# Performance work log

Hardware: AMD Instinct MI355X
Metric: run time of the kernel (lower is better)

Reference implementation:

```python
import jax, jax.numpy as jnp
import numpy as np

N_NODES = 20000
N_EDGES = 640000
D = 128            # node feature dim
NUM_HEADS = 4      # = num_irreps of edge_sh (lmax=3, 0e+1o+2e+3o)
HEAD_DIM = D // NUM_HEADS
IR_DIMS = np.array([1, 3, 5, 7])  # dims of each irrep; sum = 16
AVG_NUM_NEIGHBORS = 32.0


def setup_inputs() -> dict:
    key = jax.random.key(0)
    ks = jax.random.split(key, 20)
    inp = {
        "edge_sh": jax.random.normal(ks[0], (N_EDGES, int(IR_DIMS.sum())), jnp.float32),
        "node_feats": jax.random.normal(ks[1], (N_NODES, D), jnp.float32),
        "edge_feats": jax.random.normal(ks[2], (N_EDGES, 64), jnp.float32),
        "chi_scalar": jax.random.normal(ks[3], (N_EDGES, 64), jnp.float32),
        "cutoffs": jax.random.uniform(ks[4], (N_EDGES,), jnp.float32),
        "senders": jax.random.randint(ks[5], (N_EDGES,), 0, N_NODES),
        "receivers": jax.random.randint(ks[6], (N_EDGES,), 0, N_NODES),
        # radial MLP: 64 -> 128 -> 128 (silu between)
        "W_rad1": jax.random.normal(ks[7], (64, 128), jnp.float32) / np.sqrt(64),
        "b_rad1": jnp.zeros((128,), jnp.float32),
        "W_rad2": jax.random.normal(ks[8], (128, 128), jnp.float32) / np.sqrt(128),
        "b_rad2": jnp.zeros((128,), jnp.float32),
        # spherical-scalar MLP: 64 -> 128 -> 128
        "W_sph1": jax.random.normal(ks[9], (64, 128), jnp.float32) / np.sqrt(64),
        "b_sph1": jnp.zeros((128,), jnp.float32),
        "W_sph2": jax.random.normal(ks[10], (128, 128), jnp.float32) / np.sqrt(128),
        "b_sph2": jnp.zeros((128,), jnp.float32),
        # Q/K projections, no bias
        "Wq": jax.random.normal(ks[11], (D, D), jnp.float32) / np.sqrt(D),
        "Wk": jax.random.normal(ks[12], (D, D), jnp.float32) / np.sqrt(D),
    }
    return inp


def reference(edge_sh, node_feats, edge_feats, chi_scalar, cutoffs, senders,
              receivers, W_rad1, b_rad1, W_rad2, b_rad2, W_sph1, b_sph1,
              W_sph2, b_sph2, Wq, Wk):
    silu = jax.nn.silu
    # edge filter: radial MLP + spherical-scalar MLP
    w = silu(edge_feats @ W_rad1 + b_rad1) @ W_rad2 + b_rad2      # [E, D]
    w = w + (silu(chi_scalar @ W_sph1 + b_sph1) @ W_sph2 + b_sph2)
    w = w.reshape(-1, NUM_HEADS, HEAD_DIM)                        # [E, H, hd]
    # gathered queries/keys
    q = (node_feats @ Wq).reshape(-1, NUM_HEADS, HEAD_DIM)[receivers]
    k = (node_feats @ Wk).reshape(-1, NUM_HEADS, HEAD_DIM)[senders]
    # filter-scaled attention: per-edge, per-head scalar
    alpha = (q * w * k).sum(axis=-1) * (1.0 / np.sqrt(HEAD_DIM))  # [E, H]
    alpha = alpha * cutoffs[:, None]
    # aligned_mul: broadcast per-irrep weight over each irrep's dim (mul=1)
    y = jnp.repeat(alpha, IR_DIMS, axis=-1)                       # [E, 16]
    msg = edge_sh * y
    # scatter_sum into receivers
    chi = jax.ops.segment_sum(msg, receivers, num_segments=N_NODES)
    return chi / AVG_NUM_NEIGHBORS
```

## Files before the change

kernel.cpp:

```cpp
#include <hip/hip_runtime.h>
#include <cmath>

#define NNODES 20000
#define NEDGES 640000
#define DDIM   128
#define TN     16
#define BE     64

typedef __attribute__((ext_vector_type(8))) short bf16x8;
typedef __attribute__((ext_vector_type(4))) float f32x4;
typedef __attribute__((ext_vector_type(4))) unsigned short us4;

__device__ __forceinline__ unsigned short f2bf(float x) {
    union { float f; unsigned u; } v; v.f = x;
    unsigned r = v.u + 0x7FFFu + ((v.u >> 16) & 1u);
    return (unsigned short)(r >> 16);
}
__device__ __forceinline__ float bf2f(unsigned short h) {
    union { unsigned u; float f; } v; v.u = ((unsigned)h) << 16; return v.f;
}
__device__ __forceinline__ unsigned cvtpk(float lo, float hi) {
    unsigned r;
    asm("v_cvt_pk_bf16_f32 %0, %1, %2" : "=v"(r) : "v"(lo), "v"(hi));
    return r;
}

__global__ void pack_weights(const float* __restrict__ W, unsigned short* __restrict__ dst)
{
    const int f  = blockIdx.x;
    const int kt = f >> 3, nt = f & 7;
    const int t  = threadIdx.x;
#pragma unroll
    for (int ii = 0; ii < 2; ii++) {
        const int idx  = t * 2 + ii;
        const int lane = idx >> 3, i = idx & 7;
        const int k = kt * 32 + (lane >> 4) * 8 + i;
        const int n = nt * 16 + (lane & 15);
        dst[f * 512 + idx] = f2bf(W[k * 128 + n]);
    }
}

__global__ __launch_bounds__(256) void qk_proj_kernel(
    const float* __restrict__ nf, const float* __restrict__ Wq,
    const float* __restrict__ Wk, unsigned short* __restrict__ qbuf,
    unsigned short* __restrict__ kbuf)
{
    __shared__ float s_nf[TN * DDIM];
    const int t  = threadIdx.x;
    const int n0 = blockIdx.x * TN;
    {
        const float4* src = (const float4*)(nf + (size_t)n0 * DDIM);
        float4* dst = (float4*)s_nf;
        for (int i = t; i < TN * DDIM / 4; i += 256) dst[i] = src[i];
    }
    __syncthreads();

    const int j = t & 127;
    const float* W = (t < 128) ? Wq : Wk;
    float acc[TN];
#pragma unroll
    for (int n = 0; n < TN; n++) acc[n] = 0.f;

    for (int k = 0; k < DDIM; k += 4) {
        const float w0 = W[(k + 0) * DDIM + j];
        const float w1 = W[(k + 1) * DDIM + j];
        const float w2 = W[(k + 2) * DDIM + j];
        const float w3 = W[(k + 3) * DDIM + j];
#pragma unroll
        for (int n = 0; n < TN; n++) {
            const float4 f = *(const float4*)&s_nf[n * DDIM + k];
            acc[n] = fmaf(f.w, w3, fmaf(f.z, w2, fmaf(f.y, w1, fmaf(f.x, w0, acc[n]))));
        }
    }
    unsigned short* outp = (t < 128) ? qbuf : kbuf;
    for (int n = 0; n < TN; n++) outp[(size_t)(n0 + n) * DDIM + j] = f2bf(acc[n]);
}

__global__ __launch_bounds__(256) void edge_kernel(
    const float* __restrict__ edge_sh, const float* __restrict__ cutoffs,
    const int* __restrict__ senders, const int* __restrict__ receivers,
    const float* __restrict__ edge_feats, const float* __restrict__ chi_scalar,
    const unsigned short* __restrict__ w1r, const unsigned short* __restrict__ w1s,
    const unsigned short* __restrict__ w2r, const unsigned short* __restrict__ w2s,
    const float* __restrict__ b_rad1, const float* __restrict__ b_sph1,
    const float* __restrict__ b_rad2, const float* __restrict__ b_sph2,
    const unsigned short* __restrict__ qbuf, const unsigned short* __restrict__ kbuf,
    float* __restrict__ out)
{
    __shared__ unsigned short s_a[2 * 64 * 64];
    __shared__ unsigned short s_h[64 * 128];
    __shared__ unsigned short s_p[64 * 128];
    __shared__ float s_alpha[64][4];

    char* pa = (char*)s_a;
    char* ph = (char*)s_h;
    char* pp = (char*)s_p;

    const int t  = threadIdx.x;
    const int w  = t >> 6;
    const int l  = t & 63;
    const int eb = blockIdx.x * BE;

#pragma unroll
    for (int ii = 0; ii < 8; ii++) {
        const int e  = w * 16 + ii * 2 + (l >> 5);
        const int eg = eb + e;
        const int r  = receivers[eg];
        const int s  = senders[eg];
        const int c4 = l & 31;
        const us4 qv = *(const us4*)(qbuf + (size_t)r * 128 + c4 * 4);
        const us4 kv = *(const us4*)(kbuf + (size_t)s * 128 + c4 * 4);
        const float p0 = bf2f(qv[0]) * bf2f(kv[0]);
        const float p1 = bf2f(qv[1]) * bf2f(kv[1]);
        const float p2 = bf2f(qv[2]) * bf2f(kv[2]);
        const float p3 = bf2f(qv[3]) * bf2f(kv[3]);
        const uint2 pv = { cvtpk(p0, p1), cvtpk(p2, p3) };
        *(uint2*)(pp + ((e * 256 + c4 * 8) ^ ((e & 7) << 4))) = pv;
    }

#pragma unroll
    for (int ii = 0; ii < 4; ii++) {
        const int idx = t + ii * 256;
        const int r   = idx >> 4;
        const int c4  = idx & 15;
        const float4 a = *(const float4*)(edge_feats + (size_t)(eb + r) * 64 + c4 * 4);
        const float4 b = *(const float4*)(chi_scalar + (size_t)(eb + r) * 64 + c4 * 4);
        const uint2 av = { cvtpk(a.x, a.y), cvtpk(a.z, a.w) };
        const uint2 bv = { cvtpk(b.x, b.y), cvtpk(b.z, b.w) };
        const int off = (r * 128 + c4 * 8) ^ ((r & 7) << 4);
        *(uint2*)(pa + off)        = av;
        *(uint2*)(pa + 8192 + off) = bv;
    }
    __syncthreads();

    f32x4 acc2[2][4];
#pragma unroll
    for (int ct = 0; ct < 2; ct++)
#pragma unroll
        for (int et = 0; et < 4; et++)
            acc2[ct][et] = (f32x4){0.f, 0.f, 0.f, 0.f};

#pragma unroll
    for (int path = 0; path < 2; path++) {
        const unsigned short* W1p = path ? w1s : w1r;
        const unsigned short* W2p = path ? w2s : w2r;
        const float* b1p = path ? b_sph1 : b_rad1;
        const char*  ab  = pa + path * 8192;

        f32x4 acc1[2][4];
#pragma unroll
        for (int ht = 0; ht < 2; ht++)
#pragma unroll
            for (int et = 0; et < 4; et++)
                acc1[ht][et] = (f32x4){0.f, 0.f, 0.f, 0.f};

#pragma unroll
        for (int kt = 0; kt < 2; kt++) {
            bf16x8 bfrag[4];
#pragma unroll
            for (int et = 0; et < 4; et++) {
                const int e = et * 16 + (l & 15);
                const int k = kt * 32 + (l >> 4) * 8;
                bfrag[et] = *(const bf16x8*)(ab + ((e * 128 + k * 2) ^ ((e & 7) << 4)));
            }
#pragma unroll
            for (int ht = 0; ht < 2; ht++) {
                const int f = kt * 8 + (w * 2 + ht);
                const bf16x8 afrag = *(const bf16x8*)(W1p + (size_t)f * 512 + l * 8);
#pragma unroll
                for (int et = 0; et < 4; et++)
                    acc1[ht][et] = __builtin_amdgcn_mfma_f32_16x16x32_bf16(
                        afrag, bfrag[et], acc1[ht][et], 0, 0, 0);
            }
        }

#pragma unroll
        for (int ht = 0; ht < 2; ht++) {
            const int hid0 = w * 32 + ht * 16 + (l >> 4) * 4;
            const float4 bv = *(const float4*)(b1p + hid0);
            const float* bvf = (const float*)&bv;
#pragma unroll
            for (int et = 0; et < 4; et++) {
                const int e = et * 16 + (l & 15);
                float s[4];
#pragma unroll
                for (int r = 0; r < 4; r++) {
                    const float v = acc1[ht][et][r] + bvf[r];
                    s[r] = v * __builtin_amdgcn_rcpf(1.0f + __expf(-v));
                }
                const uint2 hv = { cvtpk(s[0], s[1]), cvtpk(s[2], s[3]) };
                *(uint2*)(ph + ((e * 256 + hid0 * 2) ^ ((e & 7) << 4))) = hv;
            }
        }
        __syncthreads();

#pragma unroll
        for (int kt = 0; kt < 4; kt++) {
            bf16x8 hfrag[4];
#pragma unroll
            for (int et = 0; et < 4; et++) {
                const int e = et * 16 + (l & 15);
                const int k = kt * 32 + (l >> 4) * 8;
                hfrag[et] = *(const bf16x8*)(ph + ((e * 256 + k * 2) ^ ((e & 7) << 4)));
            }
#pragma unroll
            for (int ct = 0; ct < 2; ct++) {
                const int f = kt * 8 + (w * 2 + ct);
                const bf16x8 afrag = *(const bf16x8*)(W2p + (size_t)f * 512 + l * 8);
#pragma unroll
                for (int et = 0; et < 4; et++)
                    acc2[ct][et] = __builtin_amdgcn_mfma_f32_16x16x32_bf16(
                        afrag, hfrag[et], acc2[ct][et], 0, 0, 0);
            }
        }
        if (path == 0) __syncthreads();
    }

    {
        f32x4 b2s[2];
#pragma unroll
        for (int ct = 0; ct < 2; ct++) {
            const int c0 = w * 32 + ct * 16 + (l >> 4) * 4;
            const float4 br = *(const float4*)(b_rad2 + c0);
            const float4 bs = *(const float4*)(b_sph2 + c0);
            b2s[ct] = (f32x4){ br.x + bs.x, br.y + bs.y, br.z + bs.z, br.w + bs.w };
        }
#pragma unroll
        for (int et = 0; et < 4; et++) {
            const int e = et * 16 + (l & 15);
            float vsum = 0.f;
#pragma unroll
            for (int ct = 0; ct < 2; ct++) {
                const int c0 = w * 32 + ct * 16 + (l >> 4) * 4;
                const us4 pv = *(const us4*)(pp + ((e * 256 + c0 * 2) ^ ((e & 7) << 4)));
#pragma unroll
                for (int r = 0; r < 4; r++)
                    vsum = fmaf(bf2f(pv[r]), acc2[ct][et][r] + b2s[ct][r], vsum);
            }
            vsum += __shfl_xor(vsum, 16, 64);
            vsum += __shfl_xor(vsum, 32, 64);
            if (l < 16) {
                s_alpha[et * 16 + l][w] = vsum * cutoffs[eb + et * 16 + l]
                                        * 0.005524271728019903f;
            }
        }
    }
    __syncthreads();

    {
        const int e   = t >> 2;
        const int c0q = t & 3;
        const int eg  = eb + e;
        const int rn  = receivers[eg];
        const float4 sh = *(const float4*)(edge_sh + (size_t)eg * 16 + c0q * 4);
        const float* shf = (const float*)&sh;
#pragma unroll
        for (int j = 0; j < 4; j++) {
            const int comp = c0q * 4 + j;
            const int head = (comp == 0) ? 0 : (comp < 4) ? 1 : (comp < 9) ? 2 : 3;
            atomicAdd(&out[(size_t)rn * 16 + comp], shf[j] * s_alpha[e][head]);
        }
    }
}

extern "C" void kernel_launch(void* const* d_in, const int* in_sizes, int n_in,
                              void* d_out, int out_size, void* d_ws, size_t ws_size,
                              hipStream_t stream)
{
    const float* edge_sh    = (const float*)d_in[0];
    const float* node_feats = (const float*)d_in[1];
    const float* edge_feats = (const float*)d_in[2];
    const float* chi_scalar = (const float*)d_in[3];
    const float* cutoffs    = (const float*)d_in[4];
    const int*   senders    = (const int*)d_in[5];
    const int*   receivers  = (const int*)d_in[6];
    const float* W_rad1 = (const float*)d_in[7];
    const float* b_rad1 = (const float*)d_in[8];
    const float* W_rad2 = (const float*)d_in[9];
    const float* b_rad2 = (const float*)d_in[10];
    const float* W_sph1 = (const float*)d_in[11];
    const float* b_sph1 = (const float*)d_in[12];
    const float* W_sph2 = (const float*)d_in[13];
    const float* b_sph2 = (const float*)d_in[14];
    const float* Wq     = (const float*)d_in[15];
    const float* Wk     = (const float*)d_in[16];

    float* out = (float*)d_out;
    unsigned short* qbuf = (unsigned short*)d_ws;
    unsigned short* kbuf = qbuf + (size_t)NNODES * DDIM;
    unsigned short* w1r  = kbuf + (size_t)NNODES * DDIM;
    unsigned short* w1s  = w1r + 16 * 512;
    unsigned short* w2r  = w1s + 16 * 512;
    unsigned short* w2s  = w2r + 32 * 512;

    hipMemsetAsync(out, 0, (size_t)out_size * sizeof(float), stream);

    pack_weights<<<16, 256, 0, stream>>>(W_rad1, w1r);
    pack_weights<<<16, 256, 0, stream>>>(W_sph1, w1s);
    pack_weights<<<32, 256, 0, stream>>>(W_rad2, w2r);
    pack_weights<<<32, 256, 0, stream>>>(W_sph2, w2s);

    qk_proj_kernel<<<NNODES / TN, 256, 0, stream>>>(node_feats, Wq, Wk, qbuf, kbuf);

    edge_kernel<<<NEDGES / BE, 256, 0, stream>>>(
        edge_sh, cutoffs, senders, receivers, edge_feats, chi_scalar,
        w1r, w1s, w2r, w2s, b_rad1, b_sph1, b_rad2, b_sph2,
        qbuf, kbuf, out);
}
```

Before: 290.3 us.

## Restructure edge kernel to one wave per 16 edges, dropping block syncs

New measurement: 396.7 us. 36.7% more time.

```diff
diff --git a/kernel.cpp b/kernel.cpp
--- a/kernel.cpp
+++ b/kernel.cpp
@@ -5,11 +5,14 @@
 #define NEDGES 640000
 #define DDIM   128
 #define TN     16
-#define BE     64
+#define BE     16
 
 typedef __attribute__((ext_vector_type(8))) short bf16x8;
 typedef __attribute__((ext_vector_type(4))) float f32x4;
 typedef __attribute__((ext_vector_type(4))) unsigned short us4;
+typedef __attribute__((ext_vector_type(8))) unsigned short us8;
+
+union U4B { uint4 u; bf16x8 b; };
 
 __device__ __forceinline__ unsigned short f2bf(float x) {
     union { float f; unsigned u; } v; v.f = x;
@@ -76,7 +79,7 @@
     for (int n = 0; n < TN; n++) outp[(size_t)(n0 + n) * DDIM + j] = f2bf(acc[n]);
 }
 
-__global__ __launch_bounds__(256) void edge_kernel(
+__global__ __launch_bounds__(64, 4) void edge_kernel(
     const float* __restrict__ edge_sh, const float* __restrict__ cutoffs,
     const int* __restrict__ senders, const int* __restrict__ receivers,
     const float* __restrict__ edge_feats, const float* __restrict__ chi_scalar,
@@ -87,178 +90,129 @@
     const unsigned short* __restrict__ qbuf, const unsigned short* __restrict__ kbuf,
     float* __restrict__ out)
 {
-    __shared__ unsigned short s_a[2 * 64 * 64];
-    __shared__ unsigned short s_h[64 * 128];
-    __shared__ unsigned short s_p[64 * 128];
-    __shared__ float s_alpha[64][4];
-
-    char* pa = (char*)s_a;
+    __shared__ unsigned short s_p[BE * 128];
+    __shared__ unsigned short s_h[BE * 128];
+    char* pp = (char*)s_p;
     char* ph = (char*)s_h;
-    char* pp = (char*)s_p;
-
-    const int t  = threadIdx.x;
-    const int w  = t >> 6;
-    const int l  = t & 63;
+
+    const int l  = threadIdx.x;
+    const int e  = l & 15;
+    const int cg = l >> 4;
     const int eb = blockIdx.x * BE;
-
-#pragma unroll
-    for (int ii = 0; ii < 8; ii++) {
-        const int e  = w * 16 + ii * 2 + (l >> 5);
-        const int eg = eb + e;
-        const int r  = receivers[eg];
-        const int s  = senders[eg];
-        const int c4 = l & 31;
-        const us4 qv = *(const us4*)(qbuf + (size_t)r * 128 + c4 * 4);
-        const us4 kv = *(const us4*)(kbuf + (size_t)s * 128 + c4 * 4);
-        const float p0 = bf2f(qv[0]) * bf2f(kv[0]);
-        const float p1 = bf2f(qv[1]) * bf2f(kv[1]);
-        const float p2 = bf2f(qv[2]) * bf2f(kv[2]);
-        const float p3 = bf2f(qv[3]) * bf2f(kv[3]);
-        const uint2 pv = { cvtpk(p0, p1), cvtpk(p2, p3) };
-        *(uint2*)(pp + ((e * 256 + c4 * 8) ^ ((e & 7) << 4))) = pv;
-    }
-
-#pragma unroll
-    for (int ii = 0; ii < 4; ii++) {
-        const int idx = t + ii * 256;
-        const int r   = idx >> 4;
-        const int c4  = idx & 15;
-        const float4 a = *(const float4*)(edge_feats + (size_t)(eb + r) * 64 + c4 * 4);
-        const float4 b = *(const float4*)(chi_scalar + (size_t)(eb + r) * 64 + c4 * 4);
-        const uint2 av = { cvtpk(a.x, a.y), cvtpk(a.z, a.w) };
-        const uint2 bv = { cvtpk(b.x, b.y), cvtpk(b.z, b.w) };
-        const int off = (r * 128 + c4 * 8) ^ ((r & 7) << 4);
-        *(uint2*)(pa + off)        = av;
-        *(uint2*)(pa + 8192 + off) = bv;
-    }
-    __syncthreads();
-
-    f32x4 acc2[2][4];
-#pragma unroll
-    for (int ct = 0; ct < 2; ct++)
-#pragma unroll
-        for (int et = 0; et < 4; et++)
-            acc2[ct][et] = (f32x4){0.f, 0.f, 0.f, 0.f};
+    const int eg = eb + e;
+    const int sw = (e & 7) << 4;
+
+    const int rn   = receivers[eg];
+    const int sn   = senders[eg];
+    const float cut = cutoffs[eg];
+
+    {
+        const unsigned short* qrow = qbuf + (size_t)rn * 128 + cg * 32;
+        const unsigned short* krow = kbuf + (size_t)sn * 128 + cg * 32;
+#pragma unroll
+        for (int j = 0; j < 4; j++) {
+            const us8 qv = *(const us8*)(qrow + j * 8);
+            const us8 kv = *(const us8*)(krow + j * 8);
+            uint4 pv;
+            pv.x = cvtpk(bf2f(qv[0]) * bf2f(kv[0]), bf2f(qv[1]) * bf2f(kv[1]));
+            pv.y = cvtpk(bf2f(qv[2]) * bf2f(kv[2]), bf2f(qv[3]) * bf2f(kv[3]));
+            pv.z = cvtpk(bf2f(qv[4]) * bf2f(kv[4]), bf2f(qv[5]) * bf2f(kv[5]));
+            pv.w = cvtpk(bf2f(qv[6]) * bf2f(kv[6]), bf2f(qv[7]) * bf2f(kv[7]));
+            *(uint4*)(pp + ((e * 256 + cg * 64 + j * 16) ^ sw)) = pv;
+        }
+    }
+
+    f32x4 acc2[8];
+#pragma unroll
+    for (int i = 0; i < 8; i++) acc2[i] = (f32x4){0.f, 0.f, 0.f, 0.f};
 
 #pragma unroll
     for (int path = 0; path < 2; path++) {
         const unsigned short* W1p = path ? w1s : w1r;
         const unsigned short* W2p = path ? w2s : w2r;
         const float* b1p = path ? b_sph1 : b_rad1;
-        const char*  ab  = pa + path * 8192;
-
-        f32x4 acc1[2][4];
-#pragma unroll
-        for (int ht = 0; ht < 2; ht++)
-#pragma unroll
-            for (int et = 0; et < 4; et++)
-                acc1[ht][et] = (f32x4){0.f, 0.f, 0.f, 0.f};
-
+        const float* inp = path ? chi_scalar : edge_feats;
+
+        bf16x8 bf1[2];
 #pragma unroll
         for (int kt = 0; kt < 2; kt++) {
-            bf16x8 bfrag[4];
-#pragma unroll
-            for (int et = 0; et < 4; et++) {
-                const int e = et * 16 + (l & 15);
-                const int k = kt * 32 + (l >> 4) * 8;
-                bfrag[et] = *(const bf16x8*)(ab + ((e * 128 + k * 2) ^ ((e & 7) << 4)));
+            const float* src = inp + (size_t)eg * 64 + kt * 32 + cg * 8;
+            const float4 a0 = *(const float4*)(src);
+            const float4 a1 = *(const float4*)(src + 4);
+            U4B u;
+            u.u.x = cvtpk(a0.x, a0.y); u.u.y = cvtpk(a0.z, a0.w);
+            u.u.z = cvtpk(a1.x, a1.y); u.u.w = cvtpk(a1.z, a1.w);
+            bf1[kt] = u.b;
+        }
+
+        f32x4 acc1[8];
+#pragma unroll
+        for (int i = 0; i < 8; i++) acc1[i] = (f32x4){0.f, 0.f, 0.f, 0.f};
+#pragma unroll
+        for (int kt = 0; kt < 2; kt++) {
+#pragma unroll
+            for (int ht = 0; ht < 8; ht++) {
+                const bf16x8 af = *(const bf16x8*)(W1p + (size_t)(kt * 8 + ht) * 512 + l * 8);
+                acc1[ht] = __builtin_amdgcn_mfma_f32_16x16x32_bf16(af, bf1[kt], acc1[ht], 0, 0, 0);
             }
-#pragma unroll
-            for (int ht = 0; ht < 2; ht++) {
-                const int f = kt * 8 + (w * 2 + ht);
-                const bf16x8 afrag = *(const bf16x8*)(W1p + (size_t)f * 512 + l * 8);
-#pragma unroll
-                for (int et = 0; et < 4; et++)
-                    acc1[ht][et] = __builtin_amdgcn_mfma_f32_16x16x32_bf16(
-                        afrag, bfrag[et], acc1[ht][et], 0, 0, 0);
-            }
-        }
-
-#pragma unroll
-        for (int ht = 0; ht < 2; ht++) {
-            const int hid0 = w * 32 + ht * 16 + (l >> 4) * 4;
+        }
+
+#pragma unroll
+        for (int ht = 0; ht < 8; ht++) {
+            const int hid0 = ht * 16 + cg * 4;
             const float4 bv = *(const float4*)(b1p + hid0);
             const float* bvf = (const float*)&bv;
-#pragma unroll
-            for (int et = 0; et < 4; et++) {
-                const int e = et * 16 + (l & 15);
-                float s[4];
-#pragma unroll
-                for (int r = 0; r < 4; r++) {
-                    const float v = acc1[ht][et][r] + bvf[r];
-                    s[r] = v * __builtin_amdgcn_rcpf(1.0f + __expf(-v));
-                }
-                const uint2 hv = { cvtpk(s[0], s[1]), cvtpk(s[2], s[3]) };
-                *(uint2*)(ph + ((e * 256 + hid0 * 2) ^ ((e & 7) << 4))) = hv;
+            float s[4];
+#pragma unroll
+            for (int r = 0; r < 4; r++) {
+                const float v = acc1[ht][r] + bvf[r];
+                s[r] = v * __builtin_amdgcn_rcpf(1.0f + __expf(-v));
             }
-        }
-        __syncthreads();
+            const uint2 hv = { cvtpk(s[0], s[1]), cvtpk(s[2], s[3]) };
+            *(uint2*)(ph + ((e * 256 + hid0 * 2) ^ sw)) = hv;
+        }
 
 #pragma unroll
         for (int kt = 0; kt < 4; kt++) {
-            bf16x8 hfrag[4];
-#pragma unroll
-            for (int et = 0; et < 4; et++) {
-                const int e = et * 16 + (l & 15);
-                const int k = kt * 32 + (l >> 4) * 8;
-                hfrag[et] = *(const bf16x8*)(ph + ((e * 256 + k * 2) ^ ((e & 7) << 4)));
+            const bf16x8 hf = *(const bf16x8*)(ph + ((e * 256 + kt * 64 + cg * 16) ^ sw));
+#pragma unroll
+            for (int ct = 0; ct < 8; ct++) {
+                const bf16x8 af = *(const bf16x8*)(W2p + (size_t)(kt * 8 + ct) * 512 + l * 8);
+                acc2[ct] = __builtin_amdgcn_mfma_f32_16x16x32_bf16(af, hf, acc2[ct], 0, 0, 0);
             }
-#pragma unroll
-            for (int ct = 0; ct < 2; ct++) {
-                const int f = kt * 8 + (w * 2 + ct);
-                const bf16x8 afrag = *(const bf16x8*)(W2p + (size_t)f * 512 + l * 8);
-#pragma unroll
-                for (int et = 0; et < 4; et++)
-                    acc2[ct][et] = __builtin_amdgcn_mfma_f32_16x16x32_bf16(
-                        afrag, hfrag[et], acc2[ct][et], 0, 0, 0);
-            }
-        }
-        if (path == 0) __syncthreads();
+        }
+    }
+
+    float vh[4] = {0.f, 0.f, 0.f, 0.f};
+#pragma unroll
+    for (int ct = 0; ct < 8; ct++) {
+        const us4 pv = *(const us4*)(pp + ((e * 256 + ct * 32 + cg * 8) ^ sw));
+        const int c0 = ct * 16 + cg * 4;
+        const float4 br = *(const float4*)(b_rad2 + c0);
+        const float4 bs = *(const float4*)(b_sph2 + c0);
+        const float* brf = (const float*)&br;
+        const float* bsf = (const float*)&bs;
+        float sum = 0.f;
+#pragma unroll
+        for (int r = 0; r < 4; r++)
+            sum = fmaf(bf2f(pv[r]), acc2[ct][r] + brf[r] + bsf[r], sum);
+        vh[ct >> 1] += sum;
+    }
+#pragma unroll
+    for (int h = 0; h < 4; h++) {
+        vh[h] += __shfl_xor(vh[h], 16, 64);
+        vh[h] += __shfl_xor(vh[h], 32, 64);
+        vh[h] *= cut * 0.005524271728019903f;
     }
 
     {
-        f32x4 b2s[2];
-#pragma unroll
-        for (int ct = 0; ct < 2; ct++) {
-            const int c0 = w * 32 + ct * 16 + (l >> 4) * 4;
-            const float4 br = *(const float4*)(b_rad2 + c0);
-            const float4 bs = *(const float4*)(b_sph2 + c0);
-            b2s[ct] = (f32x4){ br.x + bs.x, br.y + bs.y, br.z + bs.z, br.w + bs.w };
-        }
-#pragma unroll
-        for (int et = 0; et < 4; et++) {
-            const int e = et * 16 + (l & 15);
-            float vsum = 0.f;
-#pragma unroll
-            for (int ct = 0; ct < 2; ct++) {
-                const int c0 = w * 32 + ct * 16 + (l >> 4) * 4;
-                const us4 pv = *(const us4*)(pp + ((e * 256 + c0 * 2) ^ ((e & 7) << 4)));
-#pragma unroll
-                for (int r = 0; r < 4; r++)
-                    vsum = fmaf(bf2f(pv[r]), acc2[ct][et][r] + b2s[ct][r], vsum);
-            }
-            vsum += __shfl_xor(vsum, 16, 64);
-            vsum += __shfl_xor(vsum, 32, 64);
-            if (l < 16) {
-                s_alpha[et * 16 + l][w] = vsum * cutoffs[eb + et * 16 + l]
-                                        * 0.005524271728019903f;
-            }
-        }
-    }
-    __syncthreads();
-
-    {
-        const int e   = t >> 2;
-        const int c0q = t & 3;
-        const int eg  = eb + e;
-        const int rn  = receivers[eg];
-        const float4 sh = *(const float4*)(edge_sh + (size_t)eg * 16 + c0q * 4);
+        const float4 sh = *(const float4*)(edge_sh + (size_t)eg * 16 + cg * 4);
         const float* shf = (const float*)&sh;
 #pragma unroll
         for (int j = 0; j < 4; j++) {
-            const int comp = c0q * 4 + j;
+            const int comp = cg * 4 + j;
             const int head = (comp == 0) ? 0 : (comp < 4) ? 1 : (comp < 9) ? 2 : 3;
-            atomicAdd(&out[(size_t)rn * 16 + comp], shf[j] * s_alpha[e][head]);
+            atomicAdd(&out[(size_t)rn * 16 + comp], shf[j] * vh[head]);
         }
     }
 }
@@ -302,7 +256,7 @@
 
     qk_proj_kernel<<<NNODES / TN, 256, 0, stream>>>(node_feats, Wq, Wk, qbuf, kbuf);
 
-    edge_kernel<<<NEDGES / BE, 256, 0, stream>>>(
+    edge_kernel<<<NEDGES / BE, 64, 0, stream>>>(
         edge_sh, cutoffs, senders, receivers, edge_feats, chi_scalar,
         w1r, w1s, w2r, w2s, b_rad1, b_sph1, b_rad2, b_sph2,
         qbuf, kbuf, out);
```

## Split MLP paths across waves, load inputs and q/k directly into registers

Applied to the files above, without the earlier changes.

Result: slower. 389.9 us (+34.3%).

```diff
diff --git a/kernel.cpp b/kernel.cpp
--- a/kernel.cpp
+++ b/kernel.cpp
@@ -11,6 +11,8 @@
 typedef __attribute__((ext_vector_type(4))) float f32x4;
 typedef __attribute__((ext_vector_type(4))) unsigned short us4;
 
+union U4B { uint4 u; bf16x8 b; };
+
 __device__ __forceinline__ unsigned short f2bf(float x) {
     union { float f; unsigned u; } v; v.f = x;
     unsigned r = v.u + 0x7FFFu + ((v.u >> 16) & 1u);
@@ -18,6 +20,12 @@
 }
 __device__ __forceinline__ float bf2f(unsigned short h) {
     union { unsigned u; float f; } v; v.u = ((unsigned)h) << 16; return v.f;
+}
+__device__ __forceinline__ float lo2f(unsigned u) {
+    union { unsigned u; float f; } v; v.u = u << 16; return v.f;
+}
+__device__ __forceinline__ float hi2f(unsigned u) {
+    union { unsigned u; float f; } v; v.u = u & 0xffff0000u; return v.f;
 }
 __device__ __forceinline__ unsigned cvtpk(float lo, float hi) {
     unsigned r;
@@ -76,7 +84,7 @@
     for (int n = 0; n < TN; n++) outp[(size_t)(n0 + n) * DDIM + j] = f2bf(acc[n]);
 }
 
-__global__ __launch_bounds__(256) void edge_kernel(
+__global__ __launch_bounds__(256, 4) void edge_kernel(
     const float* __restrict__ edge_sh, const float* __restrict__ cutoffs,
     const int* __restrict__ senders, const int* __restrict__ receivers,
     const float* __restrict__ edge_feats, const float* __restrict__ chi_scalar,
@@ -87,162 +95,158 @@
     const unsigned short* __restrict__ qbuf, const unsigned short* __restrict__ kbuf,
     float* __restrict__ out)
 {
-    __shared__ unsigned short s_a[2 * 64 * 64];
-    __shared__ unsigned short s_h[64 * 128];
-    __shared__ unsigned short s_p[64 * 128];
+    __shared__ unsigned short s_h[64 * 256];
     __shared__ float s_alpha[64][4];
-
-    char* pa = (char*)s_a;
     char* ph = (char*)s_h;
-    char* pp = (char*)s_p;
 
     const int t  = threadIdx.x;
     const int w  = t >> 6;
     const int l  = t & 63;
+    const int el = l & 15;
+    const int rg = l >> 4;
     const int eb = blockIdx.x * BE;
 
-#pragma unroll
-    for (int ii = 0; ii < 8; ii++) {
-        const int e  = w * 16 + ii * 2 + (l >> 5);
-        const int eg = eb + e;
-        const int r  = receivers[eg];
-        const int s  = senders[eg];
-        const int c4 = l & 31;
-        const us4 qv = *(const us4*)(qbuf + (size_t)r * 128 + c4 * 4);
-        const us4 kv = *(const us4*)(kbuf + (size_t)s * 128 + c4 * 4);
-        const float p0 = bf2f(qv[0]) * bf2f(kv[0]);
-        const float p1 = bf2f(qv[1]) * bf2f(kv[1]);
-        const float p2 = bf2f(qv[2]) * bf2f(kv[2]);
-        const float p3 = bf2f(qv[3]) * bf2f(kv[3]);
-        const uint2 pv = { cvtpk(p0, p1), cvtpk(p2, p3) };
-        *(uint2*)(pp + ((e * 256 + c4 * 8) ^ ((e & 7) << 4))) = pv;
-    }
-
-#pragma unroll
-    for (int ii = 0; ii < 4; ii++) {
-        const int idx = t + ii * 256;
-        const int r   = idx >> 4;
-        const int c4  = idx & 15;
-        const float4 a = *(const float4*)(edge_feats + (size_t)(eb + r) * 64 + c4 * 4);
-        const float4 b = *(const float4*)(chi_scalar + (size_t)(eb + r) * 64 + c4 * 4);
-        const uint2 av = { cvtpk(a.x, a.y), cvtpk(a.z, a.w) };
-        const uint2 bv = { cvtpk(b.x, b.y), cvtpk(b.z, b.w) };
-        const int off = (r * 128 + c4 * 8) ^ ((r & 7) << 4);
-        *(uint2*)(pa + off)        = av;
-        *(uint2*)(pa + 8192 + off) = bv;
-    }
-    __syncthreads();
-
-    f32x4 acc2[2][4];
-#pragma unroll
-    for (int ct = 0; ct < 2; ct++)
-#pragma unroll
-        for (int et = 0; et < 4; et++)
-            acc2[ct][et] = (f32x4){0.f, 0.f, 0.f, 0.f};
-
-#pragma unroll
-    for (int path = 0; path < 2; path++) {
-        const unsigned short* W1p = path ? w1s : w1r;
-        const unsigned short* W2p = path ? w2s : w2r;
-        const float* b1p = path ? b_sph1 : b_rad1;
-        const char*  ab  = pa + path * 8192;
-
+    int rn[4], sn[4];
+    float cut[4];
+#pragma unroll
+    for (int et = 0; et < 4; et++) {
+        const int eg = eb + et * 16 + el;
+        rn[et] = receivers[eg];
+        sn[et] = senders[eg];
+        cut[et] = cutoffs[eg];
+    }
+
+    const int c0base = w * 32 + rg * 4;
+    us4 qv[2][4], kv[2][4];
+#pragma unroll
+    for (int et = 0; et < 4; et++)
+#pragma unroll
+        for (int ct = 0; ct < 2; ct++) {
+            qv[ct][et] = *(const us4*)(qbuf + (size_t)rn[et] * 128 + c0base + ct * 16);
+            kv[ct][et] = *(const us4*)(kbuf + (size_t)sn[et] * 128 + c0base + ct * 16);
+        }
+
+    const int path   = w >> 1;
+    const int ntbase = (w & 1) * 4;
+    const float* inp = path ? chi_scalar : edge_feats;
+    const unsigned short* W1p = path ? w1s : w1r;
+    const float* b1p = path ? b_sph1 : b_rad1;
+
+#pragma unroll
+    for (int nb = 0; nb < 2; nb++) {
         f32x4 acc1[2][4];
 #pragma unroll
-        for (int ht = 0; ht < 2; ht++)
+        for (int j = 0; j < 2; j++)
 #pragma unroll
             for (int et = 0; et < 4; et++)
-                acc1[ht][et] = (f32x4){0.f, 0.f, 0.f, 0.f};
+                acc1[j][et] = (f32x4){0.f, 0.f, 0.f, 0.f};
 
 #pragma unroll
         for (int kt = 0; kt < 2; kt++) {
             bf16x8 bfrag[4];
 #pragma unroll
             for (int et = 0; et < 4; et++) {
-                const int e = et * 16 + (l & 15);
-                const int k = kt * 32 + (l >> 4) * 8;
-                bfrag[et] = *(const bf16x8*)(ab + ((e * 128 + k * 2) ^ ((e & 7) << 4)));
+                const float* src = inp + (size_t)(eb + et * 16 + el) * 64 + kt * 32 + rg * 8;
+                const float4 a0 = *(const float4*)src;
+                const float4 a1 = *(const float4*)(src + 4);
+                U4B u;
+                u.u.x = cvtpk(a0.x, a0.y); u.u.y = cvtpk(a0.z, a0.w);
+                u.u.z = cvtpk(a1.x, a1.y); u.u.w = cvtpk(a1.z, a1.w);
+                bfrag[et] = u.b;
             }
 #pragma unroll
-            for (int ht = 0; ht < 2; ht++) {
-                const int f = kt * 8 + (w * 2 + ht);
-                const bf16x8 afrag = *(const bf16x8*)(W1p + (size_t)f * 512 + l * 8);
+            for (int j = 0; j < 2; j++) {
+                const int nt = ntbase + nb * 2 + j;
+                const bf16x8 af = *(const bf16x8*)(W1p + (size_t)(kt * 8 + nt) * 512 + l * 8);
 #pragma unroll
                 for (int et = 0; et < 4; et++)
-                    acc1[ht][et] = __builtin_amdgcn_mfma_f32_16x16x32_bf16(
-                        afrag, bfrag[et], acc1[ht][et], 0, 0, 0);
+                    acc1[j][et] = __builtin_amdgcn_mfma_f32_16x16x32_bf16(
+                        af, bfrag[et], acc1[j][et], 0, 0, 0);
             }
         }
 
 #pragma unroll
-        for (int ht = 0; ht < 2; ht++) {
-            const int hid0 = w * 32 + ht * 16 + (l >> 4) * 4;
-            const float4 bv = *(const float4*)(b1p + hid0);
+        for (int j = 0; j < 2; j++) {
+            const int nt = ntbase + nb * 2 + j;
+            const int hc = nt * 16 + rg * 4;
+            const float4 bv = *(const float4*)(b1p + hc);
             const float* bvf = (const float*)&bv;
 #pragma unroll
             for (int et = 0; et < 4; et++) {
-                const int e = et * 16 + (l & 15);
+                const int e = et * 16 + el;
                 float s[4];
 #pragma unroll
                 for (int r = 0; r < 4; r++) {
-                    const float v = acc1[ht][et][r] + bvf[r];
+                    const float v = acc1[j][et][r] + bvf[r];
                     s[r] = v * __builtin_amdgcn_rcpf(1.0f + __expf(-v));
                 }
                 const uint2 hv = { cvtpk(s[0], s[1]), cvtpk(s[2], s[3]) };
-                *(uint2*)(ph + ((e * 256 + hid0 * 2) ^ ((e & 7) << 4))) = hv;
+                *(uint2*)(ph + ((e * 512 + path * 256 + hc * 2) ^ ((e & 7) << 4))) = hv;
             }
         }
-        __syncthreads();
-
-#pragma unroll
-        for (int kt = 0; kt < 4; kt++) {
-            bf16x8 hfrag[4];
-#pragma unroll
-            for (int et = 0; et < 4; et++) {
-                const int e = et * 16 + (l & 15);
-                const int k = kt * 32 + (l >> 4) * 8;
-                hfrag[et] = *(const bf16x8*)(ph + ((e * 256 + k * 2) ^ ((e & 7) << 4)));
-            }
-#pragma unroll
-            for (int ct = 0; ct < 2; ct++) {
-                const int f = kt * 8 + (w * 2 + ct);
-                const bf16x8 afrag = *(const bf16x8*)(W2p + (size_t)f * 512 + l * 8);
-#pragma unroll
-                for (int et = 0; et < 4; et++)
-                    acc2[ct][et] = __builtin_amdgcn_mfma_f32_16x16x32_bf16(
-                        afrag, hfrag[et], acc2[ct][et], 0, 0, 0);
-            }
-        }
-        if (path == 0) __syncthreads();
-    }
-
-    {
-        f32x4 b2s[2];
+    }
+
+    uint2 p2[2][4];
+#pragma unroll
+    for (int ct = 0; ct < 2; ct++)
+#pragma unroll
+        for (int et = 0; et < 4; et++) {
+            const us4 q = qv[ct][et], k = kv[ct][et];
+            p2[ct][et].x = cvtpk(bf2f(q[0]) * bf2f(k[0]), bf2f(q[1]) * bf2f(k[1]));
+            p2[ct][et].y = cvtpk(bf2f(q[2]) * bf2f(k[2]), bf2f(q[3]) * bf2f(k[3]));
+        }
+    __syncthreads();
+
+    f32x4 acc2[2][4];
+#pragma unroll
+    for (int ct = 0; ct < 2; ct++)
+#pragma unroll
+        for (int et = 0; et < 4; et++)
+            acc2[ct][et] = (f32x4){0.f, 0.f, 0.f, 0.f};
+
+    f32x4 b2s[2];
+#pragma unroll
+    for (int ct = 0; ct < 2; ct++) {
+        const float4 br = *(const float4*)(b_rad2 + c0base + ct * 16);
+        const float4 bs = *(const float4*)(b_sph2 + c0base + ct * 16);
+        b2s[ct] = (f32x4){ br.x + bs.x, br.y + bs.y, br.z + bs.z, br.w + bs.w };
+    }
+
+#pragma unroll
+    for (int kt = 0; kt < 8; kt++) {
+        const unsigned short* W2p = (kt < 4) ? w2r : w2s;
+        const int fkt = kt & 3;
+        bf16x8 hfrag[4];
+#pragma unroll
+        for (int et = 0; et < 4; et++) {
+            const int e = et * 16 + el;
+            hfrag[et] = *(const bf16x8*)(ph + ((e * 512 + kt * 64 + rg * 16) ^ ((e & 7) << 4)));
+        }
 #pragma unroll
         for (int ct = 0; ct < 2; ct++) {
-            const int c0 = w * 32 + ct * 16 + (l >> 4) * 4;
-            const float4 br = *(const float4*)(b_rad2 + c0);
-            const float4 bs = *(const float4*)(b_sph2 + c0);
-            b2s[ct] = (f32x4){ br.x + bs.x, br.y + bs.y, br.z + bs.z, br.w + bs.w };
-        }
-#pragma unroll
-        for (int et = 0; et < 4; et++) {
-            const int e = et * 16 + (l & 15);
-            float vsum = 0.f;
-#pragma unroll
-            for (int ct = 0; ct < 2; ct++) {
-                const int c0 = w * 32 + ct * 16 + (l >> 4) * 4;
-                const us4 pv = *(const us4*)(pp + ((e * 256 + c0 * 2) ^ ((e & 7) << 4)));
-#pragma unroll
-                for (int r = 0; r < 4; r++)
-                    vsum = fmaf(bf2f(pv[r]), acc2[ct][et][r] + b2s[ct][r], vsum);
-            }
-            vsum += __shfl_xor(vsum, 16, 64);
-            vsum += __shfl_xor(vsum, 32, 64);
-            if (l < 16) {
-                s_alpha[et * 16 + l][w] = vsum * cutoffs[eb + et * 16 + l]
-                                        * 0.005524271728019903f;
-            }
+            const bf16x8 af = *(const bf16x8*)(W2p + (size_t)(fkt * 8 + w * 2 + ct) * 512 + l * 8);
+#pragma unroll
+            for (int et = 0; et < 4; et++)
+                acc2[ct][et] = __builtin_amdgcn_mfma_f32_16x16x32_bf16(
+                    af, hfrag[et], acc2[ct][et], 0, 0, 0);
+        }
+    }
+
+#pragma unroll
+    for (int et = 0; et < 4; et++) {
+        float vsum = 0.f;
+#pragma unroll
+        for (int ct = 0; ct < 2; ct++) {
+            const uint2 p = p2[ct][et];
+            vsum = fmaf(lo2f(p.x), acc2[ct][et][0] + b2s[ct][0], vsum);
+            vsum = fmaf(hi2f(p.x), acc2[ct][et][1] + b2s[ct][1], vsum);
+            vsum = fmaf(lo2f(p.y), acc2[ct][et][2] + b2s[ct][2], vsum);
+            vsum = fmaf(hi2f(p.y), acc2[ct][et][3] + b2s[ct][3], vsum);
+        }
+        vsum += __shfl_xor(vsum, 16, 64);
+        vsum += __shfl_xor(vsum, 32, 64);
+        if (l < 16) {
+            s_alpha[et * 16 + l][w] = vsum * cut[et] * 0.005524271728019903f;
         }
     }
     __syncthreads();
@@ -251,14 +255,14 @@
         const int e   = t >> 2;
         const int c0q = t & 3;
         const int eg  = eb + e;
-        const int rn  = receivers[eg];
+        const int rv  = receivers[eg];
         const float4 sh = *(const float4*)(edge_sh + (size_t)eg * 16 + c0q * 4);
         const float* shf = (const float*)&sh;
 #pragma unroll
         for (int j = 0; j < 4; j++) {
             const int comp = c0q * 4 + j;
             const int head = (comp == 0) ? 0 : (comp < 4) ? 1 : (comp < 9) ? 2 : 3;
-            atomicAdd(&out[(size_t)rn * 16 + comp], shf[j] * s_alpha[e][head]);
+            atomicAdd(&out[(size_t)rv * 16 + comp], shf[j] * s_alpha[e][head]);
         }
     }
 }
```

## Halve edge-kernel LDS by reusing one input buffer and prefetching chi_scalar

Applied to the files above, without the earlier changes.

After: 323.1 us. +11.3%, slower.

```diff
diff --git a/kernel.cpp b/kernel.cpp
--- a/kernel.cpp
+++ b/kernel.cpp
@@ -76,7 +76,7 @@
     for (int n = 0; n < TN; n++) outp[(size_t)(n0 + n) * DDIM + j] = f2bf(acc[n]);
 }
 
-__global__ __launch_bounds__(256) void edge_kernel(
+__global__ __launch_bounds__(256, 4) void edge_kernel(
     const float* __restrict__ edge_sh, const float* __restrict__ cutoffs,
     const int* __restrict__ senders, const int* __restrict__ receivers,
     const float* __restrict__ edge_feats, const float* __restrict__ chi_scalar,
@@ -87,18 +87,19 @@
     const unsigned short* __restrict__ qbuf, const unsigned short* __restrict__ kbuf,
     float* __restrict__ out)
 {
-    __shared__ unsigned short s_a[2 * 64 * 64];
+    __shared__ unsigned short s_a[64 * 64];
     __shared__ unsigned short s_h[64 * 128];
     __shared__ unsigned short s_p[64 * 128];
-    __shared__ float s_alpha[64][4];
-
     char* pa = (char*)s_a;
     char* ph = (char*)s_h;
     char* pp = (char*)s_p;
+    float* s_alpha = (float*)s_a;
 
     const int t  = threadIdx.x;
     const int w  = t >> 6;
     const int l  = t & 63;
+    const int el = l & 15;
+    const int rg = l >> 4;
     const int eb = blockIdx.x * BE;
 
 #pragma unroll
@@ -124,12 +125,8 @@
         const int r   = idx >> 4;
         const int c4  = idx & 15;
         const float4 a = *(const float4*)(edge_feats + (size_t)(eb + r) * 64 + c4 * 4);
-        const float4 b = *(const float4*)(chi_scalar + (size_t)(eb + r) * 64 + c4 * 4);
         const uint2 av = { cvtpk(a.x, a.y), cvtpk(a.z, a.w) };
-        const uint2 bv = { cvtpk(b.x, b.y), cvtpk(b.z, b.w) };
-        const int off = (r * 128 + c4 * 8) ^ ((r & 7) << 4);
-        *(uint2*)(pa + off)        = av;
-        *(uint2*)(pa + 8192 + off) = bv;
+        *(uint2*)(pa + ((r * 128 + c4 * 8) ^ ((r & 7) << 4))) = av;
     }
     __syncthreads();
 
@@ -140,13 +137,7 @@
         for (int et = 0; et < 4; et++)
             acc2[ct][et] = (f32x4){0.f, 0.f, 0.f, 0.f};
 
-#pragma unroll
-    for (int path = 0; path < 2; path++) {
-        const unsigned short* W1p = path ? w1s : w1r;
-        const unsigned short* W2p = path ? w2s : w2r;
-        const float* b1p = path ? b_sph1 : b_rad1;
-        const char*  ab  = pa + path * 8192;
-
+    {
         f32x4 acc1[2][4];
 #pragma unroll
         for (int ht = 0; ht < 2; ht++)
@@ -159,14 +150,14 @@
             bf16x8 bfrag[4];
 #pragma unroll
             for (int et = 0; et < 4; et++) {
-                const int e = et * 16 + (l & 15);
-                const int k = kt * 32 + (l >> 4) * 8;
-                bfrag[et] = *(const bf16x8*)(ab + ((e * 128 + k * 2) ^ ((e & 7) << 4)));
+                const int e = et * 16 + el;
+                const int k = kt * 32 + rg * 8;
+                bfrag[et] = *(const bf16x8*)(pa + ((e * 128 + k * 2) ^ ((e & 7) << 4)));
             }
 #pragma unroll
             for (int ht = 0; ht < 2; ht++) {
                 const int f = kt * 8 + (w * 2 + ht);
-                const bf16x8 afrag = *(const bf16x8*)(W1p + (size_t)f * 512 + l * 8);
+                const bf16x8 afrag = *(const bf16x8*)(w1r + (size_t)f * 512 + l * 8);
 #pragma unroll
                 for (int et = 0; et < 4; et++)
                     acc1[ht][et] = __builtin_amdgcn_mfma_f32_16x16x32_bf16(
@@ -176,12 +167,12 @@
 
 #pragma unroll
         for (int ht = 0; ht < 2; ht++) {
-            const int hid0 = w * 32 + ht * 16 + (l >> 4) * 4;
-            const float4 bv = *(const float4*)(b1p + hid0);
+            const int hid0 = w * 32 + ht * 16 + rg * 4;
+            const float4 bv = *(const float4*)(b_rad1 + hid0);
             const float* bvf = (const float*)&bv;
 #pragma unroll
             for (int et = 0; et < 4; et++) {
-                const int e = et * 16 + (l & 15);
+                const int e = et * 16 + el;
                 float s[4];
 #pragma unroll
                 for (int r = 0; r < 4; r++) {
@@ -194,44 +185,131 @@
         }
         __syncthreads();
 
+        float4 chv[4];
+#pragma unroll
+        for (int ii = 0; ii < 4; ii++) {
+            const int idx = t + ii * 256;
+            const int r   = idx >> 4;
+            const int c4  = idx & 15;
+            chv[ii] = *(const float4*)(chi_scalar + (size_t)(eb + r) * 64 + c4 * 4);
+        }
+
 #pragma unroll
         for (int kt = 0; kt < 4; kt++) {
             bf16x8 hfrag[4];
 #pragma unroll
             for (int et = 0; et < 4; et++) {
-                const int e = et * 16 + (l & 15);
-                const int k = kt * 32 + (l >> 4) * 8;
+                const int e = et * 16 + el;
+                const int k = kt * 32 + rg * 8;
                 hfrag[et] = *(const bf16x8*)(ph + ((e * 256 + k * 2) ^ ((e & 7) << 4)));
             }
 #pragma unroll
             for (int ct = 0; ct < 2; ct++) {
                 const int f = kt * 8 + (w * 2 + ct);
-                const bf16x8 afrag = *(const bf16x8*)(W2p + (size_t)f * 512 + l * 8);
+                const bf16x8 afrag = *(const bf16x8*)(w2r + (size_t)f * 512 + l * 8);
 #pragma unroll
                 for (int et = 0; et < 4; et++)
                     acc2[ct][et] = __builtin_amdgcn_mfma_f32_16x16x32_bf16(
                         afrag, hfrag[et], acc2[ct][et], 0, 0, 0);
             }
         }
-        if (path == 0) __syncthreads();
-    }
-
-    {
+
+#pragma unroll
+        for (int ii = 0; ii < 4; ii++) {
+            const int idx = t + ii * 256;
+            const int r   = idx >> 4;
+            const int c4  = idx & 15;
+            const uint2 bv = { cvtpk(chv[ii].x, chv[ii].y), cvtpk(chv[ii].z, chv[ii].w) };
+            *(uint2*)(pa + ((r * 128 + c4 * 8) ^ ((r & 7) << 4))) = bv;
+        }
+        __syncthreads();
+    }
+
+    {
+        f32x4 acc1[2][4];
+#pragma unroll
+        for (int ht = 0; ht < 2; ht++)
+#pragma unroll
+            for (int et = 0; et < 4; et++)
+                acc1[ht][et] = (f32x4){0.f, 0.f, 0.f, 0.f};
+
+#pragma unroll
+        for (int kt = 0; kt < 2; kt++) {
+            bf16x8 bfrag[4];
+#pragma unroll
+            for (int et = 0; et < 4; et++) {
+                const int e = et * 16 + el;
+                const int k = kt * 32 + rg * 8;
+                bfrag[et] = *(const bf16x8*)(pa + ((e * 128 + k * 2) ^ ((e & 7) << 4)));
+            }
+#pragma unroll
+            for (int ht = 0; ht < 2; ht++) {
+                const int f = kt * 8 + (w * 2 + ht);
+                const bf16x8 afrag = *(const bf16x8*)(w1s + (size_t)f * 512 + l * 8);
+#pragma unroll
+                for (int et = 0; et < 4; et++)
+                    acc1[ht][et] = __builtin_amdgcn_mfma_f32_16x16x32_bf16(
+                        afrag, bfrag[et], acc1[ht][et], 0, 0, 0);
+            }
+        }
+
+#pragma unroll
+        for (int ht = 0; ht < 2; ht++) {
+            const int hid0 = w * 32 + ht * 16 + rg * 4;
+            const float4 bv = *(const float4*)(b_sph1 + hid0);
+            const float* bvf = (const float*)&bv;
+#pragma unroll
+            for (int et = 0; et < 4; et++) {
+                const int e = et * 16 + el;
+                float s[4];
+#pragma unroll
+                for (int r = 0; r < 4; r++) {
+                    const float v = acc1[ht][et][r] + bvf[r];
+                    s[r] = v * __builtin_amdgcn_rcpf(1.0f + __expf(-v));
+                }
+                const uint2 hv = { cvtpk(s[0], s[1]), cvtpk(s[2], s[3]) };
+                *(uint2*)(ph + ((e * 256 + hid0 * 2) ^ ((e & 7) << 4))) = hv;
+            }
+        }
+        __syncthreads();
+
+#pragma unroll
+        for (int kt = 0; kt < 4; kt++) {
+            bf16x8 hfrag[4];
+#pragma unroll
+            for (int et = 0; et < 4; et++) {
+                const int e = et * 16 + el;
+                const int k = kt * 32 + rg * 8;
+                hfrag[et] = *(const bf16x8*)(ph + ((e * 256 + k * 2) ^ ((e & 7) << 4)));
+            }
+#pragma unroll
+            for (int ct = 0; ct < 2; ct++) {
+                const int f = kt * 8 + (w * 2 + ct);
+                const bf16x8 afrag = *(const bf16x8*)(w2s + (size_t)f * 512 + l * 8);
+#pragma unroll
+                for (int et = 0; et < 4; et++)
+                    acc2[ct][et] = __builtin_amdgcn_mfma_f32_16x16x32_bf16(
+                        afrag, hfrag[et], acc2[ct][et], 0, 0, 0);
+            }
+        }
+    }
+
+    {
+        const int c0base = w * 32 + rg * 4;
         f32x4 b2s[2];
 #pragma unroll
         for (int ct = 0; ct < 2; ct++) {
-            const int c0 = w * 32 + ct * 16 + (l >> 4) * 4;
-            const float4 br = *(const float4*)(b_rad2 + c0);
-            const float4 bs = *(const float4*)(b_sph2 + c0);
+            const float4 br = *(const float4*)(b_rad2 + c0base + ct * 16);
+            const float4 bs = *(const float4*)(b_sph2 + c0base + ct * 16);
             b2s[ct] = (f32x4){ br.x + bs.x, br.y + bs.y, br.z + bs.z, br.w + bs.w };
         }
 #pragma unroll
         for (int et = 0; et < 4; et++) {
-            const int e = et * 16 + (l & 15);
+            const int e = et * 16 + el;
             float vsum = 0.f;
 #pragma unroll
             for (int ct = 0; ct < 2; ct++) {
-                const int c0 = w * 32 + ct * 16 + (l >> 4) * 4;
+                const int c0 = c0base + ct * 16;
                 const us4 pv = *(const us4*)(pp + ((e * 256 + c0 * 2) ^ ((e & 7) << 4)));
 #pragma unroll
                 for (int r = 0; r < 4; r++)
@@ -240,8 +318,8 @@
             vsum += __shfl_xor(vsum, 16, 64);
             vsum += __shfl_xor(vsum, 32, 64);
             if (l < 16) {
-                s_alpha[et * 16 + l][w] = vsum * cutoffs[eb + et * 16 + l]
-                                        * 0.005524271728019903f;
+                s_alpha[(et * 16 + l) * 4 + w] = vsum * cutoffs[eb + et * 16 + l]
+                                               * 0.005524271728019903f;
             }
         }
     }
@@ -251,14 +329,14 @@
         const int e   = t >> 2;
         const int c0q = t & 3;
         const int eg  = eb + e;
-        const int rn  = receivers[eg];
+        const int rv  = receivers[eg];
         const float4 sh = *(const float4*)(edge_sh + (size_t)eg * 16 + c0q * 4);
         const float* shf = (const float*)&sh;
 #pragma unroll
         for (int j = 0; j < 4; j++) {
             const int comp = c0q * 4 + j;
             const int head = (comp == 0) ? 0 : (comp < 4) ? 1 : (comp < 9) ? 2 : 3;
-            atomicAdd(&out[(size_t)rn * 16 + comp], shf[j] * s_alpha[e][head]);
+            atomicAdd(&out[(size_t)rv * 16 + comp], shf[j] * s_alpha[e * 4 + head]);
         }
     }
 }
```
